# Performance work log

Measured on AMD Instinct MI355X. Metric: run time of the kernel, lower is better.

Reference implementation:

```python
import jax, jax.numpy as jnp
import numpy as np

N_SPEC = 300
N_MEAS = 9
BATCH = 131072
N_LAYERS = 5

def soft_thresh(v, t):
    return jnp.sign(v) * jnp.maximum(jnp.abs(v) - t, 0.0)

def setup_inputs() -> dict:
    key = jax.random.key(0)
    k1, k2, k3 = jax.random.split(key, 3)
    b = jax.random.normal(k1, (BATCH, N_MEAS), dtype=jnp.float32)
    target = jax.random.normal(k2, (BATCH, N_SPEC), dtype=jnp.float32)
    A = jax.random.uniform(k3, (N_MEAS, N_SPEC), dtype=jnp.float32)
    gamma_tv = jnp.full((N_LAYERS,), 5.0, dtype=jnp.float32)
    lambda_tv = jnp.full((N_LAYERS,), 0.001, dtype=jnp.float32)
    alpha = jnp.full((N_LAYERS,), 5.0, dtype=jnp.float32)
    return {"b": b, "target": target, "A": A,
            "gamma_tv": gamma_tv, "lambda_tv": lambda_tv, "alpha": alpha}

def reference(b, target, A, gamma_tv, lambda_tv, alpha):
    n = A.shape[1]
    I = jnp.eye(n, dtype=A.dtype)
    Delta = jnp.roll(I, 1, axis=1) - I            # [n, n]
    DtD = Delta.T @ Delta                          # [n, n]
    ATA = A.T @ A                                  # [n, n]
    bA = b @ A                                     # [batch, n], constant across layers

    x = jnp.ones_like(target)
    eta_tv = jnp.zeros_like(x)
    tau = jnp.zeros_like(x)

    for i in range(N_LAYERS):
        g, lam, al = gamma_tv[i], lambda_tv[i], alpha[i]
        # u_tv: soft-threshold of circular TV differences
        delta_x = jnp.roll(x, 1, axis=1) - x
        u_tv = soft_thresh(delta_x + eta_tv / g, lam / g)
        # w: nonneg projection
        w = jnp.maximum(x + tau / al, 0.0)
        # x-update: solve via small matrix inverse (as in original)
        residual = bA + al * w - tau + g * u_tv - eta_tv      # [batch, n]
        add_item = ATA + al * I + g * DtD                     # [n, n]
        x = residual @ jnp.linalg.inv(add_item)
        # dual updates
        eta_tv = eta_tv + g * (x @ Delta - u_tv)
        tau = tau + al * (x - w)
    return x
```

## Files before the change

### kernel.cpp

```cpp
#include <hip/hip_runtime.h>
#include <math.h>

#define NS 300
#define NM 9
#define NB 131072
#define NL 5
#define GPITCH 320

#define OFF_C 0
#define OFF_G 1536
#define OFF_H 15360

__global__ void k_cinv(const float* __restrict__ alpha,
                       const float* __restrict__ gamma,
                       float* __restrict__ cbuf) {
  __shared__ double costab[NS];
  __shared__ double invlam[NS];
  const int l = blockIdx.x;
  const int j = threadIdx.x;
  const double al = (double)alpha[l], g = (double)gamma[l];
  const double tpn = 6.283185307179586476925286766559 / (double)NS;
  if (j < NS) {
    double cj = cos(tpn * (double)j);
    costab[j] = cj;
    invlam[j] = 1.0 / (al + 2.0 * g * (1.0 - cj));
  }
  __syncthreads();
  if (j < NS) {
    double s = 0.0;
    for (int m = 0; m < NS; ++m) s += costab[(j * m) % NS] * invlam[m];
    cbuf[l * NS + j] = (float)(s / (double)NS);
  }
}

__global__ void k_G(const float* __restrict__ A, const float* __restrict__ cbuf,
                    float* __restrict__ Gbuf) {
  const int l = blockIdx.x / NM, kk = blockIdx.x % NM;
  const int j = threadIdx.x;
  if (j >= NS) return;
  const float* c = cbuf + l * NS;
  const float* Ak = A + kk * NS;
  float s = 0.f;
  for (int i = 0; i < NS; ++i) {
    int d = i - j; if (d < 0) d += NS;
    s = fmaf(Ak[i], c[d], s);
  }
  Gbuf[(l * NM + kk) * NS + j] = s;
}

__global__ void k_SH(const float* __restrict__ A, const float* __restrict__ Gbuf,
                     float* __restrict__ Hbuf) {
  __shared__ float Si[9][18];
  const int l = blockIdx.x, t = threadIdx.x;
  const float* G = Gbuf + l * NM * NS;
  if (t < 81) {
    int p = t / 9, q = t % 9;
    float s = (p == q) ? 1.f : 0.f;
    const float* Gp = G + p * NS;
    const float* Aq = A + q * NS;
    for (int j = 0; j < NS; ++j) s = fmaf(Gp[j], Aq[j], s);
    Si[p][q] = s;
    Si[p][q + 9] = (p == q) ? 1.f : 0.f;
  }
  __syncthreads();
  if (t == 0) {
    for (int p = 0; p < 9; ++p) {
      float piv = 1.f / Si[p][p];
      for (int q = 0; q < 18; ++q) Si[p][q] *= piv;
      for (int r = 0; r < 9; ++r) if (r != p) {
        float f = Si[r][p];
        for (int q = 0; q < 18; ++q) Si[r][q] -= f * Si[p][q];
      }
    }
  }
  __syncthreads();
  for (int idx = t; idx < NM * NS; idx += blockDim.x) {
    int p = idx / NS, j = idx % NS;
    float s = 0.f;
    #pragma unroll
    for (int q = 0; q < 9; ++q) s = fmaf(Si[p][q + 9], G[q * NS + j], s);
    Hbuf[l * NM * NS + idx] = s;
  }
}

__global__ __launch_bounds__(256, 4)
void k_main(const float* __restrict__ b, const float* __restrict__ A,
            const float* __restrict__ gam, const float* __restrict__ lamv,
            const float* __restrict__ alp,
            const float* __restrict__ Gbuf, const float* __restrict__ Hbuf,
            float* __restrict__ out) {
  __shared__ float Gl[NM * GPITCH];
  __shared__ float Hl[NM * GPITCH];

  const int tid = threadIdx.x;
  const int tx = tid & 63;
  const int wv = tid >> 6;
  const int col = tx * 5;
  const bool live = (tx < 60);
  const int prevlane = (tx == 0) ? 59 : (tx - 1);
  const int row0 = blockIdx.x * 8 + wv * 2;

  if (tid < 180) {
    int q = tid / 20, j2 = 300 + (tid % 20);
    Gl[q * GPITCH + j2] = 0.f;
    Hl[q * GPITCH + j2] = 0.f;
  }

  float x[2][5], eta[2][5], tau[2][5], z[2][5], y[2][5], bA[2][5];
  #pragma unroll
  for (int r = 0; r < 2; ++r)
    #pragma unroll
    for (int c = 0; c < 5; ++c) { x[r][c] = 1.f; eta[r][c] = 0.f; tau[r][c] = 0.f; bA[r][c] = 0.f; }

  #pragma unroll
  for (int r = 0; r < 2; ++r) {
    float bb0[NM];
    #pragma unroll
    for (int k = 0; k < NM; ++k) bb0[k] = b[(size_t)(row0 + r) * NM + k];
    if (live) {
      #pragma unroll
      for (int c = 0; c < 5; ++c) {
        float s = 0.f;
        #pragma unroll
        for (int k = 0; k < NM; ++k) s = fmaf(bb0[k], A[k * NS + col + c], s);
        bA[r][c] = s;
      }
    }
  }

  for (int l = 0; l < NL; ++l) {
    const float g = gam[l], lm = lamv[l], al = alp[l];
    const float ig = 1.f / g, ia = 1.f / al, thr = lm * ig;
    const float m2 = al + 2.f * g;
    const float disc = sqrtf(fmaxf(fmaf(m2, m2, -4.f * g * g), 0.f));
    float rho = (m2 - disc) / (2.f * g);
    rho = fmaxf(rho, 1e-30f);
    const float Kc = 1.f / disc;
    const float rp2 = rho * rho, rp3 = rp2 * rho, rp4 = rp2 * rp2, rp5 = rp4 * rho;
    const float l2r = log2f(rho);
    const float rcf = exp2f((float)col * l2r);
    const float rcb = exp2f((float)(295 - col) * l2r);

    __syncthreads();

    {
      const float* Gg = Gbuf + l * NM * NS;
      const float* Hg = Hbuf + l * NM * NS;
      for (int i = tid; i < (NM * NS) / 4; i += 256) {
        int q = i / 75, jj = (i % 75) * 4;
        *(float4*)&Gl[q * GPITCH + jj] = *(const float4*)&Gg[q * NS + jj];
        *(float4*)&Hl[q * GPITCH + jj] = *(const float4*)&Hg[q * NS + jj];
      }
    }

    #pragma unroll
    for (int r = 0; r < 2; ++r) {
      float xp = __shfl(x[r][4], prevlane, 64);
      #pragma unroll
      for (int c = 0; c < 5; ++c) {
        float xl = (c == 0) ? xp : x[r][c - 1];
        float v = (xl - x[r][c]) + eta[r][c] * ig;
        float av = fabsf(v) - thr;
        float uu = (av > 0.f) ? copysignf(av, v) : 0.f;
        float ww = fmaf(tau[r][c], ia, x[r][c]);
        ww = (ww > 0.f) ? ww : 0.f;
        float awv = al * ww;
        float yv = bA[r][c] + awv - tau[r][c] + g * uu - eta[r][c];
        y[r][c] = live ? yv : 0.f;
        z[r][c] = fmaf(-g, uu, eta[r][c]);
      }
    }

    float acc[2][5];
    #pragma unroll
    for (int r = 0; r < 2; ++r) {
      float f0 = y[r][0];
      float f1 = fmaf(rho, f0, y[r][1]);
      float f2 = fmaf(rho, f1, y[r][2]);
      float f3 = fmaf(rho, f2, y[r][3]);
      float f4 = fmaf(rho, f3, y[r][4]);
      float cf = f4;
      float rw = rp5;
      #pragma unroll
      for (int d = 1; d <= 32; d <<= 1) {
        float t = __shfl_up(cf, d, 64);
        cf = fmaf((tx >= d) ? rw : 0.f, t, cf);
        rw *= rw;
      }
      float Ef = __shfl_up(cf, 1, 64);
      Ef = (tx >= 1) ? Ef : 0.f;
      float Fe = __shfl(cf, 59, 64);
      Ef = fmaf(rcf, Fe, Ef);

      float g4 = y[r][4];
      float g3 = fmaf(rho, g4, y[r][3]);
      float g2 = fmaf(rho, g3, y[r][2]);
      float g1 = fmaf(rho, g2, y[r][1]);
      float g0 = fmaf(rho, g1, y[r][0]);
      float cb = g0;
      rw = rp5;
      #pragma unroll
      for (int d = 1; d <= 32; d <<= 1) {
        float t = __shfl_down(cb, d, 64);
        cb = fmaf((tx <= 63 - d) ? rw : 0.f, t, cb);
        rw *= rw;
      }
      float Eb = __shfl_down(cb, 1, 64);
      Eb = (tx <= 62) ? Eb : 0.f;
      float Be = __shfl(cb, 0, 64);
      Eb = fmaf(rcb, Be, Eb);

      f0 = fmaf(rho, Ef, f0);  g0 = fmaf(rp5, Eb, g0);
      f1 = fmaf(rp2, Ef, f1);  g1 = fmaf(rp4, Eb, g1);
      f2 = fmaf(rp3, Ef, f2);  g2 = fmaf(rp3, Eb, g2);
      f3 = fmaf(rp4, Ef, f3);  g3 = fmaf(rp2, Eb, g3);
      f4 = fmaf(rp5, Ef, f4);  g4 = fmaf(rho, Eb, g4);

      acc[r][0] = Kc * ((f0 + g0) - y[r][0]);
      acc[r][1] = Kc * ((f1 + g1) - y[r][1]);
      acc[r][2] = Kc * ((f2 + g2) - y[r][2]);
      acc[r][3] = Kc * ((f3 + g3) - y[r][3]);
      acc[r][4] = Kc * ((f4 + g4) - y[r][4]);
    }

    __syncthreads();

    #pragma unroll
    for (int qg = 0; qg < NM; qg += 3) {
      float p00 = 0.f, p01 = 0.f, p02 = 0.f, p10 = 0.f, p11 = 0.f, p12 = 0.f;
      #pragma unroll
      for (int c = 0; c < 5; ++c) {
        float gv0 = Gl[(qg + 0) * GPITCH + col + c];
        float gv1 = Gl[(qg + 1) * GPITCH + col + c];
        float gv2 = Gl[(qg + 2) * GPITCH + col + c];
        p00 = fmaf(y[0][c], gv0, p00); p10 = fmaf(y[1][c], gv0, p10);
        p01 = fmaf(y[0][c], gv1, p01); p11 = fmaf(y[1][c], gv1, p11);
        p02 = fmaf(y[0][c], gv2, p02); p12 = fmaf(y[1][c], gv2, p12);
      }
      #pragma unroll
      for (int m = 32; m >= 1; m >>= 1) {
        p00 += __shfl_xor(p00, m, 64);
        p01 += __shfl_xor(p01, m, 64);
        p02 += __shfl_xor(p02, m, 64);
        p10 += __shfl_xor(p10, m, 64);
        p11 += __shfl_xor(p11, m, 64);
        p12 += __shfl_xor(p12, m, 64);
      }
      #pragma unroll
      for (int c = 0; c < 5; ++c) {
        float h0 = Hl[(qg + 0) * GPITCH + col + c];
        float h1 = Hl[(qg + 1) * GPITCH + col + c];
        float h2 = Hl[(qg + 2) * GPITCH + col + c];
        acc[0][c] = fmaf(-p00, h0, acc[0][c]);
        acc[1][c] = fmaf(-p10, h0, acc[1][c]);
        acc[0][c] = fmaf(-p01, h1, acc[0][c]);
        acc[1][c] = fmaf(-p11, h1, acc[1][c]);
        acc[0][c] = fmaf(-p02, h2, acc[0][c]);
        acc[1][c] = fmaf(-p12, h2, acc[1][c]);
      }
    }

    #pragma unroll
    for (int r = 0; r < 2; ++r) {
      #pragma unroll
      for (int c = 0; c < 5; ++c) x[r][c] = acc[r][c];
      float xp = __shfl(x[r][4], prevlane, 64);
      #pragma unroll
      for (int c = 0; c < 5; ++c) {
        float xl = (c == 0) ? xp : x[r][c - 1];
        eta[r][c] = fmaf(g, xl - x[r][c], z[r][c]);
        tau[r][c] = fmaf(al, x[r][c], (bA[r][c] - y[r][c]) - z[r][c]);
      }
    }
  }

  if (live) {
    #pragma unroll
    for (int r = 0; r < 2; ++r) {
      size_t o = (size_t)(row0 + r) * NS + col;
      #pragma unroll
      for (int c = 0; c < 5; ++c) out[o + c] = x[r][c];
    }
  }
}

extern "C" void kernel_launch(void* const* d_in, const int* in_sizes, int n_in,
                              void* d_out, int out_size, void* d_ws, size_t ws_size,
                              hipStream_t stream) {
  const float* b   = (const float*)d_in[0];
  const float* A   = (const float*)d_in[2];
  const float* gam = (const float*)d_in[3];
  const float* lm  = (const float*)d_in[4];
  const float* al  = (const float*)d_in[5];
  float* out = (float*)d_out;
  float* ws  = (float*)d_ws;

  float* cbuf = ws + OFF_C;
  float* Gbuf = ws + OFF_G;
  float* Hbuf = ws + OFF_H;

  k_cinv<<<dim3(NL), dim3(320), 0, stream>>>(al, gam, cbuf);
  k_G   <<<dim3(NL * NM), dim3(320), 0, stream>>>(A, cbuf, Gbuf);
  k_SH  <<<dim3(NL), dim3(128), 0, stream>>>(A, Gbuf, Hbuf);
  k_main<<<dim3(NB / 8), dim3(256), 0, stream>>>(b, A, gam, lm, al,
                                                 Gbuf, Hbuf, out);
}
```

Before: 912.8 us.

## Apply low-rank correction via A on circulant solve output; drop LDS staging

The Woodbury correction now projects the circulant-solved vector through A directly instead of projecting the raw residual through the precomputed G, so G no longer has to be staged. The per-layer LDS copies of G and H and both block barriers are removed; A and H are read straight from global memory and served by cache. The prefix-scan shuffle steps are cut from six to four, since the rho powers decay below float precision after about sixteen lanes. This trades shared-memory traffic and barriers for scattered global loads and a truncation that depends on rho being small.

```diff
diff --git a/kernel.cpp b/kernel.cpp
--- a/kernel.cpp
+++ b/kernel.cpp
@@ -5,7 +5,6 @@
 #define NM 9
 #define NB 131072
 #define NL 5
-#define GPITCH 320
 
 #define OFF_C 0
 #define OFF_G 1536
@@ -87,24 +86,15 @@
 void k_main(const float* __restrict__ b, const float* __restrict__ A,
             const float* __restrict__ gam, const float* __restrict__ lamv,
             const float* __restrict__ alp,
-            const float* __restrict__ Gbuf, const float* __restrict__ Hbuf,
-            float* __restrict__ out) {
-  __shared__ float Gl[NM * GPITCH];
-  __shared__ float Hl[NM * GPITCH];
-
+            const float* __restrict__ Hbuf, float* __restrict__ out) {
   const int tid = threadIdx.x;
   const int tx = tid & 63;
   const int wv = tid >> 6;
   const int col = tx * 5;
   const bool live = (tx < 60);
+  const int colc = live ? col : 0;
   const int prevlane = (tx == 0) ? 59 : (tx - 1);
   const int row0 = blockIdx.x * 8 + wv * 2;
-
-  if (tid < 180) {
-    int q = tid / 20, j2 = 300 + (tid % 20);
-    Gl[q * GPITCH + j2] = 0.f;
-    Hl[q * GPITCH + j2] = 0.f;
-  }
 
   float x[2][5], eta[2][5], tau[2][5], z[2][5], y[2][5], bA[2][5];
   #pragma unroll
@@ -140,18 +130,7 @@
     const float l2r = log2f(rho);
     const float rcf = exp2f((float)col * l2r);
     const float rcb = exp2f((float)(295 - col) * l2r);
-
-    __syncthreads();
-
-    {
-      const float* Gg = Gbuf + l * NM * NS;
-      const float* Hg = Hbuf + l * NM * NS;
-      for (int i = tid; i < (NM * NS) / 4; i += 256) {
-        int q = i / 75, jj = (i % 75) * 4;
-        *(float4*)&Gl[q * GPITCH + jj] = *(const float4*)&Gg[q * NS + jj];
-        *(float4*)&Hl[q * GPITCH + jj] = *(const float4*)&Hg[q * NS + jj];
-      }
-    }
+    const float* Hg = Hbuf + l * NM * NS;
 
     #pragma unroll
     for (int r = 0; r < 2; ++r) {
@@ -164,14 +143,13 @@
         float uu = (av > 0.f) ? copysignf(av, v) : 0.f;
         float ww = fmaf(tau[r][c], ia, x[r][c]);
         ww = (ww > 0.f) ? ww : 0.f;
-        float awv = al * ww;
-        float yv = bA[r][c] + awv - tau[r][c] + g * uu - eta[r][c];
+        float yv = bA[r][c] + al * ww - tau[r][c] + g * uu - eta[r][c];
         y[r][c] = live ? yv : 0.f;
         z[r][c] = fmaf(-g, uu, eta[r][c]);
       }
     }
 
-    float acc[2][5];
+    float xc[2][5];
     #pragma unroll
     for (int r = 0; r < 2; ++r) {
       float f0 = y[r][0];
@@ -182,7 +160,7 @@
       float cf = f4;
       float rw = rp5;
       #pragma unroll
-      for (int d = 1; d <= 32; d <<= 1) {
+      for (int d = 1; d <= 8; d <<= 1) {
         float t = __shfl_up(cf, d, 64);
         cf = fmaf((tx >= d) ? rw : 0.f, t, cf);
         rw *= rw;
@@ -200,7 +178,7 @@
       float cb = g0;
       rw = rp5;
       #pragma unroll
-      for (int d = 1; d <= 32; d <<= 1) {
+      for (int d = 1; d <= 8; d <<= 1) {
         float t = __shfl_down(cb, d, 64);
         cb = fmaf((tx <= 63 - d) ? rw : 0.f, t, cb);
         rw *= rw;
@@ -216,26 +194,30 @@
       f3 = fmaf(rp4, Ef, f3);  g3 = fmaf(rp2, Eb, g3);
       f4 = fmaf(rp5, Ef, f4);  g4 = fmaf(rho, Eb, g4);
 
-      acc[r][0] = Kc * ((f0 + g0) - y[r][0]);
-      acc[r][1] = Kc * ((f1 + g1) - y[r][1]);
-      acc[r][2] = Kc * ((f2 + g2) - y[r][2]);
-      acc[r][3] = Kc * ((f3 + g3) - y[r][3]);
-      acc[r][4] = Kc * ((f4 + g4) - y[r][4]);
-    }
-
-    __syncthreads();
+      xc[r][0] = live ? (Kc * ((f0 + g0) - y[r][0])) : 0.f;
+      xc[r][1] = live ? (Kc * ((f1 + g1) - y[r][1])) : 0.f;
+      xc[r][2] = live ? (Kc * ((f2 + g2) - y[r][2])) : 0.f;
+      xc[r][3] = live ? (Kc * ((f3 + g3) - y[r][3])) : 0.f;
+      xc[r][4] = live ? (Kc * ((f4 + g4) - y[r][4])) : 0.f;
+    }
+
+    float acc[2][5];
+    #pragma unroll
+    for (int r = 0; r < 2; ++r)
+      #pragma unroll
+      for (int c = 0; c < 5; ++c) acc[r][c] = xc[r][c];
 
     #pragma unroll
     for (int qg = 0; qg < NM; qg += 3) {
       float p00 = 0.f, p01 = 0.f, p02 = 0.f, p10 = 0.f, p11 = 0.f, p12 = 0.f;
       #pragma unroll
       for (int c = 0; c < 5; ++c) {
-        float gv0 = Gl[(qg + 0) * GPITCH + col + c];
-        float gv1 = Gl[(qg + 1) * GPITCH + col + c];
-        float gv2 = Gl[(qg + 2) * GPITCH + col + c];
-        p00 = fmaf(y[0][c], gv0, p00); p10 = fmaf(y[1][c], gv0, p10);
-        p01 = fmaf(y[0][c], gv1, p01); p11 = fmaf(y[1][c], gv1, p11);
-        p02 = fmaf(y[0][c], gv2, p02); p12 = fmaf(y[1][c], gv2, p12);
+        float a0 = A[(qg + 0) * NS + colc + c];
+        float a1 = A[(qg + 1) * NS + colc + c];
+        float a2 = A[(qg + 2) * NS + colc + c];
+        p00 = fmaf(xc[0][c], a0, p00); p10 = fmaf(xc[1][c], a0, p10);
+        p01 = fmaf(xc[0][c], a1, p01); p11 = fmaf(xc[1][c], a1, p11);
+        p02 = fmaf(xc[0][c], a2, p02); p12 = fmaf(xc[1][c], a2, p12);
       }
       #pragma unroll
       for (int m = 32; m >= 1; m >>= 1) {
@@ -248,9 +230,9 @@
       }
       #pragma unroll
       for (int c = 0; c < 5; ++c) {
-        float h0 = Hl[(qg + 0) * GPITCH + col + c];
-        float h1 = Hl[(qg + 1) * GPITCH + col + c];
-        float h2 = Hl[(qg + 2) * GPITCH + col + c];
+        float h0 = Hg[(qg + 0) * NS + colc + c];
+        float h1 = Hg[(qg + 1) * NS + colc + c];
+        float h2 = Hg[(qg + 2) * NS + colc + c];
         acc[0][c] = fmaf(-p00, h0, acc[0][c]);
         acc[1][c] = fmaf(-p10, h0, acc[1][c]);
         acc[0][c] = fmaf(-p01, h1, acc[0][c]);
@@ -303,5 +285,5 @@
   k_G   <<<dim3(NL * NM), dim3(320), 0, stream>>>(A, cbuf, Gbuf);
   k_SH  <<<dim3(NL), dim3(128), 0, stream>>>(A, Gbuf, Hbuf);
   k_main<<<dim3(NB / 8), dim3(256), 0, stream>>>(b, A, gam, lm, al,
-                                                 Gbuf, Hbuf, out);
-}
+                                                 Hbuf, out);
+}
```

Result: slower. 1.186 ms (+29.9%).
